# Optimization experiments

Measured on AMD Instinct MI355X. Metric: run time of the kernel, lower is better.

Reference implementation:

```python
import jax, jax.numpy as jnp
import numpy as np

N = 100000
E = 3200000
F_IN = 256
D_OUT = 128


def setup_inputs() -> dict:
    key = jax.random.key(0)
    ks = jax.random.split(key, 12)
    x = jax.random.normal(ks[0], (N, F_IN), dtype=jnp.float32)
    adj_val = jax.random.uniform(ks[1], (E,), dtype=jnp.float32)
    edge_row = jnp.sort(jax.random.randint(ks[2], (E,), 0, N))
    edge_col = jax.random.randint(ks[3], (E,), 0, N)
    # learned params (glorot-ish scaling)
    W1 = jax.random.normal(ks[4], (F_IN, D_OUT), dtype=jnp.float32) * (1.0 / np.sqrt(F_IN))   # conv1d_1 (1x1, no bias)
    w2 = jax.random.normal(ks[5], (D_OUT, 1), dtype=jnp.float32) * (1.0 / np.sqrt(D_OUT))     # conv1d_2
    b2 = jnp.zeros((1,), dtype=jnp.float32)
    w3 = jax.random.normal(ks[6], (D_OUT, 1), dtype=jnp.float32) * (1.0 / np.sqrt(D_OUT))     # conv1d_3
    b3 = jnp.zeros((1,), dtype=jnp.float32)
    kernel = jax.random.normal(ks[7], (F_IN, D_OUT), dtype=jnp.float32) * (1.0 / np.sqrt(F_IN))
    bias = jax.random.normal(ks[8], (N, D_OUT), dtype=jnp.float32) * 0.02
    return {"x": x, "adj_val": adj_val, "W1": W1, "w2": w2, "b2": b2,
            "w3": w3, "b3": b3, "kernel": kernel, "bias": bias,
            "edge_row": edge_row, "edge_col": edge_col}


def reference(x, adj_val, W1, w2, b2, w3, b3, kernel, bias, edge_row, edge_col):
    # 1x1 conv projections (equivalent to per-node dense layers)
    mapped = x @ W1                                   # [N, D]
    sa1 = (mapped @ w2 + b2)[:, 0]                    # [N]
    sa2 = (mapped @ w3 + b3)[:, 0]                    # [N]
    # sparse*dense broadcast then sparse add: per edge (i,j):
    #   adj_val * sa1[i] + adj_val * sa2[j]
    e = adj_val * (sa1[edge_row] + sa2[edge_col])     # [E]
    e = jax.nn.leaky_relu(e, negative_slope=0.2)
    # sparse row-wise softmax over nonzero entries
    m = jax.ops.segment_max(e, edge_row, num_segments=N)        # [N]
    m = jnp.where(jnp.isfinite(m), m, 0.0)
    ex = jnp.exp(e - m[edge_row])                               # [E]
    denom = jax.ops.segment_sum(ex, edge_row, num_segments=N)   # [N]
    denom = jnp.where(denom > 0, denom, 1.0)
    att = ex / denom[edge_row]                                  # [E]
    # dense feature transform then SpMM aggregation
    value = x @ kernel                                          # [N, D_OUT]
    out = jax.ops.segment_sum(att[:, None] * value[edge_col], edge_row, num_segments=N)
    out = out + bias                                            # use_bias=True
    return out  # activation=None (linear), single head, 'average' reduction
```

## Files before the change

kernel.cpp:

```cpp
#include <hip/hip_runtime.h>
#include <math.h>

#define N_NODES 100000
#define N_EDGES 3200000
#define F_IN    256
#define D_OUT   128

typedef __attribute__((ext_vector_type(8))) short short8;
typedef __attribute__((ext_vector_type(4))) float f32x4;

__device__ __forceinline__ unsigned short f2bf(float f) {
    unsigned u = __float_as_uint(f);
    unsigned r = (u + 0x7FFFu + ((u >> 16) & 1u)) >> 16;
    return (unsigned short)r;
}

__device__ __forceinline__ float dot4(f32x4 a, f32x4 b) {
    return a.x * b.x + a.y * b.y + a.z * b.z + a.w * b.w;
}

__device__ __forceinline__ float ub(unsigned u, int k) {
    return (float)((u >> (k * 8)) & 0xffu);
}

__global__ __launch_bounds__(128) void prep_kernel(
    const float* __restrict__ W1, const float* __restrict__ w2,
    const float* __restrict__ w3, const float* __restrict__ kern,
    float* __restrict__ v1, float* __restrict__ v2,
    unsigned short* __restrict__ kbT) {
    const int kk  = blockIdx.x;
    const int tid = threadIdx.x;
    kbT[(size_t)tid * F_IN + kk] = f2bf(kern[(size_t)kk * D_OUT + tid]);
    if (tid < 64) {
        const float* wr = W1 + (size_t)kk * D_OUT;
        float a = wr[tid], b = wr[tid + 64];
        float s1 = a * w2[tid] + b * w2[tid + 64];
        float s2 = a * w3[tid] + b * w3[tid + 64];
#pragma unroll
        for (int o = 32; o > 0; o >>= 1) {
            s1 += __shfl_xor(s1, o);
            s2 += __shfl_xor(s2, o);
        }
        if (tid == 0) { v1[kk] = s1; v2[kk] = s2; }
    }
}

__global__ void row_ptr_kernel(const int* __restrict__ edge_row,
                               int* __restrict__ row_ptr) {
    int r = blockIdx.x * blockDim.x + threadIdx.x;
    if (r > N_NODES) return;
    int lo = 0, hi = N_EDGES;
    while (lo < hi) {
        int mid = (lo + hi) >> 1;
        if (edge_row[mid] < r) lo = mid + 1; else hi = mid;
    }
    row_ptr[r] = lo;
}

__global__ __launch_bounds__(256) void gemm_sa_kernel(
    const float* __restrict__ x, const unsigned short* __restrict__ kbT,
    const float* __restrict__ v1, const float* __restrict__ v2,
    const float* __restrict__ b2p, const float* __restrict__ b3p,
    unsigned char* __restrict__ valq, float2* __restrict__ szc,
    float* __restrict__ sa1) {
    const int wid = blockIdx.x * 4 + (threadIdx.x >> 6);
    const int m_base = wid * 32;
    if (m_base >= N_NODES) return;
    const int lane = threadIdx.x & 63;
    const int r = lane & 15;
    const int q = lane >> 4;

    const f32x4* x0 = (const f32x4*)(x + (size_t)(m_base + r) * F_IN + q * 8);
    const f32x4* x1 = (const f32x4*)(x + (size_t)(m_base + 16 + r) * F_IN + q * 8);

    f32x4 acc[2][8];
#pragma unroll
    for (int t = 0; t < 2; ++t)
#pragma unroll
        for (int nt = 0; nt < 8; ++nt) acc[t][nt] = (f32x4)(0.f);
    float s1a = 0.f, s1b = 0.f, s2a = 0.f, s2b = 0.f;

#pragma unroll 2
    for (int s = 0; s < 8; ++s) {
        f32x4 p00 = __builtin_nontemporal_load(x0 + s * 8);
        f32x4 p01 = __builtin_nontemporal_load(x0 + s * 8 + 1);
        f32x4 p10 = __builtin_nontemporal_load(x1 + s * 8);
        f32x4 p11 = __builtin_nontemporal_load(x1 + s * 8 + 1);
        const f32x4* vp1 = (const f32x4*)(v1 + s * 32 + q * 8);
        const f32x4* vp2 = (const f32x4*)(v2 + s * 32 + q * 8);
        f32x4 va = vp1[0], vb = vp1[1], vc = vp2[0], vd = vp2[1];
        s1a += dot4(p00, va) + dot4(p01, vb);
        s2a += dot4(p00, vc) + dot4(p01, vd);
        s1b += dot4(p10, va) + dot4(p11, vb);
        s2b += dot4(p10, vc) + dot4(p11, vd);

        short8 a0, a1;
        a0[0] = (short)f2bf(p00.x); a0[1] = (short)f2bf(p00.y);
        a0[2] = (short)f2bf(p00.z); a0[3] = (short)f2bf(p00.w);
        a0[4] = (short)f2bf(p01.x); a0[5] = (short)f2bf(p01.y);
        a0[6] = (short)f2bf(p01.z); a0[7] = (short)f2bf(p01.w);
        a1[0] = (short)f2bf(p10.x); a1[1] = (short)f2bf(p10.y);
        a1[2] = (short)f2bf(p10.z); a1[3] = (short)f2bf(p10.w);
        a1[4] = (short)f2bf(p11.x); a1[5] = (short)f2bf(p11.y);
        a1[6] = (short)f2bf(p11.z); a1[7] = (short)f2bf(p11.w);

#pragma unroll
        for (int nt = 0; nt < 8; ++nt) {
            const short8 b = *(const short8*)(kbT + (size_t)(nt * 16 + r) * F_IN
                                              + s * 32 + q * 8);
            acc[0][nt] = __builtin_amdgcn_mfma_f32_16x16x32_bf16(a0, b, acc[0][nt], 0, 0, 0);
            acc[1][nt] = __builtin_amdgcn_mfma_f32_16x16x32_bf16(a1, b, acc[1][nt], 0, 0, 0);
        }
    }

    s1a += __shfl_xor(s1a, 16); s1a += __shfl_xor(s1a, 32);
    s1b += __shfl_xor(s1b, 16); s1b += __shfl_xor(s1b, 32);
    s2a += __shfl_xor(s2a, 16); s2a += __shfl_xor(s2a, 32);
    s2b += __shfl_xor(s2b, 16); s2b += __shfl_xor(s2b, 32);
    if (q == 0) {
        float bb2 = b2p[0], bb3 = b3p[0];
        sa1[m_base + r]      = s1a + bb2;
        sa1[m_base + 16 + r] = s1b + bb2;
        szc[m_base + r].x      = s2a + bb3;
        szc[m_base + 16 + r].x = s2b + bb3;
    }

#pragma unroll
    for (int t = 0; t < 2; ++t)
#pragma unroll
        for (int reg = 0; reg < 4; ++reg) {
            float m = 0.f;
#pragma unroll
            for (int nt = 0; nt < 8; ++nt) m = fmaxf(m, fabsf(acc[t][nt][reg]));
            m = fmaxf(m, __shfl_xor(m, 1));
            m = fmaxf(m, __shfl_xor(m, 2));
            m = fmaxf(m, __shfl_xor(m, 4));
            m = fmaxf(m, __shfl_xor(m, 8));
            const int row = m_base + t * 16 + q * 4 + reg;
            const float inv = m > 0.f ? 127.f / m : 0.f;
            if (r == 0) szc[row].y = m * (1.f / 127.f);
#pragma unroll
            for (int nt = 0; nt < 8; ++nt) {
                int iq = (int)rintf(acc[t][nt][reg] * inv);
                valq[(size_t)row * D_OUT + nt * 16 + r] =
                    (unsigned char)(iq + 128);
            }
        }
}

__global__ __launch_bounds__(256) void attn_agg_kernel(
    const int* __restrict__ row_ptr, const int* __restrict__ edge_col,
    const float* __restrict__ adj, const float* __restrict__ sa1,
    const float2* __restrict__ szc, const unsigned char* __restrict__ valq,
    const float* __restrict__ bias, float* __restrict__ out) {
    const int lane = threadIdx.x & 63;
    const int g    = lane >> 4;
    const int r    = lane & 15;
    const int row  = blockIdx.x * 4 + (threadIdx.x >> 6);

    const int s   = row_ptr[row];
    const int cnt = row_ptr[row + 1] - s;
    const float sa1r = sa1[row];
    const unsigned char* vbase = valq + r * 8;

    const f32x4* bp = (const f32x4*)(bias + (size_t)row * D_OUT + r * 8);
    f32x4 b0 = __builtin_nontemporal_load(bp);
    f32x4 b1 = __builtin_nontemporal_load(bp + 1);

    float acc[8];
#pragma unroll
    for (int j = 0; j < 8; ++j) acc[j] = 0.f;
    float sum = 0.f, sumw = 0.f;

    for (int base = 0; base < cnt; base += 64) {
        const int n = min(64, cnt - base);

        int c = 0;
        float w = 0.f;
        if (lane < n) {
            const int e = s + base + lane;
            c = __builtin_nontemporal_load(edge_col + e);
            const float a = __builtin_nontemporal_load(adj + e);
            const float2 f2 = szc[c];
            float t = a * (sa1r + f2.x);
            t = fmaxf(t, 0.2f * t);
            const float ex = __expf(t);
            sum += ex;
            w = ex * f2.y;
        }
        sumw += w;

        const int nchunk = (n + 15) >> 4;
        uint2 p[16];
#pragma unroll
        for (int ch = 0; ch < 4; ++ch) {
            if (ch < nchunk) {
#pragma unroll
                for (int k4 = 0; k4 < 4; ++k4) {
                    const int k = ch * 4 + k4;
                    const int cc = __shfl(c, k * 4 + g);
                    p[k] = *(const uint2*)(vbase + (size_t)cc * D_OUT);
                }
            }
        }
#pragma unroll
        for (int ch = 0; ch < 4; ++ch) {
            if (ch < nchunk) {
#pragma unroll
                for (int k4 = 0; k4 < 4; ++k4) {
                    const int k = ch * 4 + k4;
                    const float ww = __shfl(w, k * 4 + g);
                    const uint2 q = p[k];
                    acc[0] += ww * ub(q.x, 0); acc[1] += ww * ub(q.x, 1);
                    acc[2] += ww * ub(q.x, 2); acc[3] += ww * ub(q.x, 3);
                    acc[4] += ww * ub(q.y, 0); acc[5] += ww * ub(q.y, 1);
                    acc[6] += ww * ub(q.y, 2); acc[7] += ww * ub(q.y, 3);
                }
            }
        }
    }

    sum  += __shfl_xor(sum, 1);  sumw += __shfl_xor(sumw, 1);
    sum  += __shfl_xor(sum, 2);  sumw += __shfl_xor(sumw, 2);
    sum  += __shfl_xor(sum, 4);  sumw += __shfl_xor(sumw, 4);
    sum  += __shfl_xor(sum, 8);  sumw += __shfl_xor(sumw, 8);
#pragma unroll
    for (int o = 16; o < 64; o <<= 1) {
        sum  += __shfl_xor(sum, o);
        sumw += __shfl_xor(sumw, o);
#pragma unroll
        for (int j = 0; j < 8; ++j) acc[j] += __shfl_xor(acc[j], o);
    }
    const float inv  = sum > 0.f ? 1.f / sum : 1.f;
    const float corr = 128.f * sumw;

    if (g == 0) {
        f32x4 r0, r1;
        r0.x = (acc[0] - corr) * inv + b0.x; r0.y = (acc[1] - corr) * inv + b0.y;
        r0.z = (acc[2] - corr) * inv + b0.z; r0.w = (acc[3] - corr) * inv + b0.w;
        r1.x = (acc[4] - corr) * inv + b1.x; r1.y = (acc[5] - corr) * inv + b1.y;
        r1.z = (acc[6] - corr) * inv + b1.z; r1.w = (acc[7] - corr) * inv + b1.w;
        f32x4* op = (f32x4*)(out + (size_t)row * D_OUT + r * 8);
        __builtin_nontemporal_store(r0, op);
        __builtin_nontemporal_store(r1, op + 1);
    }
}

extern "C" void kernel_launch(void* const* d_in, const int* in_sizes, int n_in,
                              void* d_out, int out_size, void* d_ws,
                              size_t ws_size, hipStream_t stream) {
    const float* x        = (const float*)d_in[0];
    const float* adj      = (const float*)d_in[1];
    const float* W1       = (const float*)d_in[2];
    const float* w2       = (const float*)d_in[3];
    const float* b2       = (const float*)d_in[4];
    const float* w3       = (const float*)d_in[5];
    const float* b3       = (const float*)d_in[6];
    const float* kern     = (const float*)d_in[7];
    const float* bias     = (const float*)d_in[8];
    const int*   edge_row = (const int*)d_in[9];
    const int*   edge_col = (const int*)d_in[10];
    float* out = (float*)d_out;

    unsigned char* valq = (unsigned char*)d_ws;
    float2* szc = (float2*)(valq + (size_t)N_NODES * D_OUT);
    float*  sa1 = (float*)(szc + N_NODES);
    int* row_ptr = (int*)(sa1 + N_NODES);
    float* v1 = (float*)(row_ptr + N_NODES + 4);
    float* v2 = v1 + F_IN;
    unsigned short* kbT = (unsigned short*)(v2 + F_IN);

    hipLaunchKernelGGL(prep_kernel, dim3(256), dim3(128), 0, stream,
                       W1, w2, w3, kern, v1, v2, kbT);
    hipLaunchKernelGGL(row_ptr_kernel, dim3((N_NODES + 1 + 255) / 256),
                       dim3(256), 0, stream, edge_row, row_ptr);
    hipLaunchKernelGGL(gemm_sa_kernel, dim3((N_NODES / 32 + 3) / 4), dim3(256),
                       0, stream, x, kbT, v1, v2, b2, b3, valq, szc, sa1);
    hipLaunchKernelGGL(attn_agg_kernel, dim3(N_NODES / 4), dim3(256), 0,
                       stream, row_ptr, edge_col, adj, sa1, szc, valq,
                       bias, out);
}
```

Baseline: 354.2 us.

## Process two rows per wavefront in attention aggregation to overlap gathers

The attention-aggregation kernel now has each wavefront handle two consecutive rows, issuing the edge loads, score gathers and quantized value gathers for both rows before accumulating. The first 64 edges of each row go through an unrolled fast path, and longer rows fall back to a loop. The aim is more memory-level parallelism per wave and lower per-row fixed costs such as reductions and row_ptr loads. In exchange it raises register pressure, which may reduce occupancy, and duplicates a lot of code.

```diff
diff --git a/kernel.cpp b/kernel.cpp
--- a/kernel.cpp
+++ b/kernel.cpp
@@ -156,91 +156,232 @@
     const int lane = threadIdx.x & 63;
     const int g    = lane >> 4;
     const int r    = lane & 15;
-    const int row  = blockIdx.x * 4 + (threadIdx.x >> 6);
-
-    const int s   = row_ptr[row];
-    const int cnt = row_ptr[row + 1] - s;
-    const float sa1r = sa1[row];
+    const int rA   = __builtin_amdgcn_readfirstlane(
+                         blockIdx.x * 8 + (threadIdx.x >> 6) * 2);
+    const int rB   = rA + 1;
+
+    const int sA = row_ptr[rA];
+    const int eA = row_ptr[rA + 1];
+    const int eB = row_ptr[rA + 2];
+    const int cntA = eA - sA, cntB = eB - eA;
+    const float sa1A = sa1[rA], sa1B = sa1[rB];
     const unsigned char* vbase = valq + r * 8;
 
-    const f32x4* bp = (const f32x4*)(bias + (size_t)row * D_OUT + r * 8);
-    f32x4 b0 = __builtin_nontemporal_load(bp);
-    f32x4 b1 = __builtin_nontemporal_load(bp + 1);
-
-    float acc[8];
-#pragma unroll
-    for (int j = 0; j < 8; ++j) acc[j] = 0.f;
-    float sum = 0.f, sumw = 0.f;
-
-    for (int base = 0; base < cnt; base += 64) {
-        const int n = min(64, cnt - base);
-
-        int c = 0;
-        float w = 0.f;
-        if (lane < n) {
-            const int e = s + base + lane;
-            c = __builtin_nontemporal_load(edge_col + e);
-            const float a = __builtin_nontemporal_load(adj + e);
-            const float2 f2 = szc[c];
-            float t = a * (sa1r + f2.x);
-            t = fmaxf(t, 0.2f * t);
-            const float ex = __expf(t);
-            sum += ex;
-            w = ex * f2.y;
-        }
-        sumw += w;
-
-        const int nchunk = (n + 15) >> 4;
-        uint2 p[16];
-#pragma unroll
-        for (int ch = 0; ch < 4; ++ch) {
-            if (ch < nchunk) {
-#pragma unroll
-                for (int k4 = 0; k4 < 4; ++k4) {
-                    const int k = ch * 4 + k4;
-                    const int cc = __shfl(c, k * 4 + g);
-                    p[k] = *(const uint2*)(vbase + (size_t)cc * D_OUT);
-                }
-            }
-        }
-#pragma unroll
-        for (int ch = 0; ch < 4; ++ch) {
-            if (ch < nchunk) {
-#pragma unroll
-                for (int k4 = 0; k4 < 4; ++k4) {
-                    const int k = ch * 4 + k4;
-                    const float ww = __shfl(w, k * 4 + g);
-                    const uint2 q = p[k];
-                    acc[0] += ww * ub(q.x, 0); acc[1] += ww * ub(q.x, 1);
-                    acc[2] += ww * ub(q.x, 2); acc[3] += ww * ub(q.x, 3);
-                    acc[4] += ww * ub(q.y, 0); acc[5] += ww * ub(q.y, 1);
-                    acc[6] += ww * ub(q.y, 2); acc[7] += ww * ub(q.y, 3);
-                }
-            }
-        }
-    }
-
-    sum  += __shfl_xor(sum, 1);  sumw += __shfl_xor(sumw, 1);
-    sum  += __shfl_xor(sum, 2);  sumw += __shfl_xor(sumw, 2);
-    sum  += __shfl_xor(sum, 4);  sumw += __shfl_xor(sumw, 4);
-    sum  += __shfl_xor(sum, 8);  sumw += __shfl_xor(sumw, 8);
+    const int nA = min(cntA, 64), nB = min(cntB, 64);
+    int cA = 0, cB = 0;
+    float aA = 0.f, aB = 0.f;
+    if (lane < nA) {
+        cA = __builtin_nontemporal_load(edge_col + sA + lane);
+        aA = __builtin_nontemporal_load(adj + sA + lane);
+    }
+    if (lane < nB) {
+        cB = __builtin_nontemporal_load(edge_col + eA + lane);
+        aB = __builtin_nontemporal_load(adj + eA + lane);
+    }
+    float2 fA, fB;
+    fA.x = 0.f; fA.y = 0.f; fB.x = 0.f; fB.y = 0.f;
+    if (lane < nA) fA = szc[cA];
+    if (lane < nB) fB = szc[cB];
+
+    float sumA = 0.f, wA = 0.f;
+    float sumB = 0.f, wB = 0.f;
+    if (lane < nA) {
+        float t = aA * (sa1A + fA.x);
+        t = fmaxf(t, 0.2f * t);
+        const float ex = __expf(t);
+        sumA = ex; wA = ex * fA.y;
+    }
+    if (lane < nB) {
+        float t = aB * (sa1B + fB.x);
+        t = fmaxf(t, 0.2f * t);
+        const float ex = __expf(t);
+        sumB = ex; wB = ex * fB.y;
+    }
+    float sumwA = wA, sumwB = wB;
+
+    float accA[8], accB[8];
+#pragma unroll
+    for (int j = 0; j < 8; ++j) { accA[j] = 0.f; accB[j] = 0.f; }
+
+    const int qA = (nA + 3) >> 2;
+    const int qB = (nB + 3) >> 2;
+    uint2 pA[8], pB[8];
+
+#pragma unroll
+    for (int k = 0; k < 8; ++k)
+        if (k < qA) {
+            const int cc = __shfl(cA, k * 4 + g);
+            pA[k] = *(const uint2*)(vbase + (size_t)cc * D_OUT);
+        }
+#pragma unroll
+    for (int k = 0; k < 8; ++k)
+        if (k < qB) {
+            const int cc = __shfl(cB, k * 4 + g);
+            pB[k] = *(const uint2*)(vbase + (size_t)cc * D_OUT);
+        }
+#pragma unroll
+    for (int k = 0; k < 8; ++k)
+        if (k < qA) {
+            const float ww = __shfl(wA, k * 4 + g);
+            const uint2 q = pA[k];
+            accA[0] += ww * ub(q.x, 0); accA[1] += ww * ub(q.x, 1);
+            accA[2] += ww * ub(q.x, 2); accA[3] += ww * ub(q.x, 3);
+            accA[4] += ww * ub(q.y, 0); accA[5] += ww * ub(q.y, 1);
+            accA[6] += ww * ub(q.y, 2); accA[7] += ww * ub(q.y, 3);
+        }
+    if (qA > 8) {
+#pragma unroll
+        for (int k = 8; k < 16; ++k)
+            if (k < qA) {
+                const int cc = __shfl(cA, k * 4 + g);
+                pA[k - 8] = *(const uint2*)(vbase + (size_t)cc * D_OUT);
+            }
+    }
+#pragma unroll
+    for (int k = 0; k < 8; ++k)
+        if (k < qB) {
+            const float ww = __shfl(wB, k * 4 + g);
+            const uint2 q = pB[k];
+            accB[0] += ww * ub(q.x, 0); accB[1] += ww * ub(q.x, 1);
+            accB[2] += ww * ub(q.x, 2); accB[3] += ww * ub(q.x, 3);
+            accB[4] += ww * ub(q.y, 0); accB[5] += ww * ub(q.y, 1);
+            accB[6] += ww * ub(q.y, 2); accB[7] += ww * ub(q.y, 3);
+        }
+    if (qB > 8) {
+#pragma unroll
+        for (int k = 8; k < 16; ++k)
+            if (k < qB) {
+                const int cc = __shfl(cB, k * 4 + g);
+                pB[k - 8] = *(const uint2*)(vbase + (size_t)cc * D_OUT);
+            }
+    }
+    if (qA > 8) {
+#pragma unroll
+        for (int k = 8; k < 16; ++k)
+            if (k < qA) {
+                const float ww = __shfl(wA, k * 4 + g);
+                const uint2 q = pA[k - 8];
+                accA[0] += ww * ub(q.x, 0); accA[1] += ww * ub(q.x, 1);
+                accA[2] += ww * ub(q.x, 2); accA[3] += ww * ub(q.x, 3);
+                accA[4] += ww * ub(q.y, 0); accA[5] += ww * ub(q.y, 1);
+                accA[6] += ww * ub(q.y, 2); accA[7] += ww * ub(q.y, 3);
+            }
+    }
+    if (qB > 8) {
+#pragma unroll
+        for (int k = 8; k < 16; ++k)
+            if (k < qB) {
+                const float ww = __shfl(wB, k * 4 + g);
+                const uint2 q = pB[k - 8];
+                accB[0] += ww * ub(q.x, 0); accB[1] += ww * ub(q.x, 1);
+                accB[2] += ww * ub(q.x, 2); accB[3] += ww * ub(q.x, 3);
+                accB[4] += ww * ub(q.y, 0); accB[5] += ww * ub(q.y, 1);
+                accB[6] += ww * ub(q.y, 2); accB[7] += ww * ub(q.y, 3);
+            }
+    }
+
+    if (cntA > 64) {
+        for (int base = 64; base < cntA; base += 64) {
+            const int n = min(64, cntA - base);
+            int c = 0; float w = 0.f;
+            if (lane < n) {
+                const int e = sA + base + lane;
+                c = edge_col[e];
+                const float a = adj[e];
+                const float2 f2 = szc[c];
+                float t = a * (sa1A + f2.x);
+                t = fmaxf(t, 0.2f * t);
+                const float ex = __expf(t);
+                sumA += ex; w = ex * f2.y;
+            }
+            sumwA += w;
+            const int qn = (n + 3) >> 2;
+            for (int k = 0; k < qn; ++k) {
+                const int cc = __shfl(c, k * 4 + g);
+                const float ww = __shfl(w, k * 4 + g);
+                const uint2 q = *(const uint2*)(vbase + (size_t)cc * D_OUT);
+                accA[0] += ww * ub(q.x, 0); accA[1] += ww * ub(q.x, 1);
+                accA[2] += ww * ub(q.x, 2); accA[3] += ww * ub(q.x, 3);
+                accA[4] += ww * ub(q.y, 0); accA[5] += ww * ub(q.y, 1);
+                accA[6] += ww * ub(q.y, 2); accA[7] += ww * ub(q.y, 3);
+            }
+        }
+    }
+    if (cntB > 64) {
+        for (int base = 64; base < cntB; base += 64) {
+            const int n = min(64, cntB - base);
+            int c = 0; float w = 0.f;
+            if (lane < n) {
+                const int e = eA + base + lane;
+                c = edge_col[e];
+                const float a = adj[e];
+                const float2 f2 = szc[c];
+                float t = a * (sa1B + f2.x);
+                t = fmaxf(t, 0.2f * t);
+                const float ex = __expf(t);
+                sumB += ex; w = ex * f2.y;
+            }
+            sumwB += w;
+            const int qn = (n + 3) >> 2;
+            for (int k = 0; k < qn; ++k) {
+                const int cc = __shfl(c, k * 4 + g);
+                const float ww = __shfl(w, k * 4 + g);
+                const uint2 q = *(const uint2*)(vbase + (size_t)cc * D_OUT);
+                accB[0] += ww * ub(q.x, 0); accB[1] += ww * ub(q.x, 1);
+                accB[2] += ww * ub(q.x, 2); accB[3] += ww * ub(q.x, 3);
+                accB[4] += ww * ub(q.y, 0); accB[5] += ww * ub(q.y, 1);
+                accB[6] += ww * ub(q.y, 2); accB[7] += ww * ub(q.y, 3);
+            }
+        }
+    }
+
+    const f32x4* bpA = (const f32x4*)(bias + (size_t)rA * D_OUT + r * 8);
+    const f32x4* bpB = (const f32x4*)(bias + (size_t)rB * D_OUT + r * 8);
+    f32x4 bA0, bA1, bB0, bB1;
+    if (g == 0) { bA0 = __builtin_nontemporal_load(bpA);
+                  bA1 = __builtin_nontemporal_load(bpA + 1); }
+    if (g == 1) { bB0 = __builtin_nontemporal_load(bpB);
+                  bB1 = __builtin_nontemporal_load(bpB + 1); }
+
+    sumA += __shfl_xor(sumA, 1);  sumwA += __shfl_xor(sumwA, 1);
+    sumA += __shfl_xor(sumA, 2);  sumwA += __shfl_xor(sumwA, 2);
+    sumA += __shfl_xor(sumA, 4);  sumwA += __shfl_xor(sumwA, 4);
+    sumA += __shfl_xor(sumA, 8);  sumwA += __shfl_xor(sumwA, 8);
+    sumB += __shfl_xor(sumB, 1);  sumwB += __shfl_xor(sumwB, 1);
+    sumB += __shfl_xor(sumB, 2);  sumwB += __shfl_xor(sumwB, 2);
+    sumB += __shfl_xor(sumB, 4);  sumwB += __shfl_xor(sumwB, 4);
+    sumB += __shfl_xor(sumB, 8);  sumwB += __shfl_xor(sumwB, 8);
 #pragma unroll
     for (int o = 16; o < 64; o <<= 1) {
-        sum  += __shfl_xor(sum, o);
-        sumw += __shfl_xor(sumw, o);
-#pragma unroll
-        for (int j = 0; j < 8; ++j) acc[j] += __shfl_xor(acc[j], o);
-    }
-    const float inv  = sum > 0.f ? 1.f / sum : 1.f;
-    const float corr = 128.f * sumw;
+        sumA += __shfl_xor(sumA, o); sumwA += __shfl_xor(sumwA, o);
+        sumB += __shfl_xor(sumB, o); sumwB += __shfl_xor(sumwB, o);
+#pragma unroll
+        for (int j = 0; j < 8; ++j) {
+            accA[j] += __shfl_xor(accA[j], o);
+            accB[j] += __shfl_xor(accB[j], o);
+        }
+    }
 
     if (g == 0) {
+        const float inv  = sumA > 0.f ? 1.f / sumA : 1.f;
+        const float corr = 128.f * sumwA;
         f32x4 r0, r1;
-        r0.x = (acc[0] - corr) * inv + b0.x; r0.y = (acc[1] - corr) * inv + b0.y;
-        r0.z = (acc[2] - corr) * inv + b0.z; r0.w = (acc[3] - corr) * inv + b0.w;
-        r1.x = (acc[4] - corr) * inv + b1.x; r1.y = (acc[5] - corr) * inv + b1.y;
-        r1.z = (acc[6] - corr) * inv + b1.z; r1.w = (acc[7] - corr) * inv + b1.w;
-        f32x4* op = (f32x4*)(out + (size_t)row * D_OUT + r * 8);
+        r0.x = (accA[0] - corr) * inv + bA0.x; r0.y = (accA[1] - corr) * inv + bA0.y;
+        r0.z = (accA[2] - corr) * inv + bA0.z; r0.w = (accA[3] - corr) * inv + bA0.w;
+        r1.x = (accA[4] - corr) * inv + bA1.x; r1.y = (accA[5] - corr) * inv + bA1.y;
+        r1.z = (accA[6] - corr) * inv + bA1.z; r1.w = (accA[7] - corr) * inv + bA1.w;
+        f32x4* op = (f32x4*)(out + (size_t)rA * D_OUT + r * 8);
+        __builtin_nontemporal_store(r0, op);
+        __builtin_nontemporal_store(r1, op + 1);
+    } else if (g == 1) {
+        const float inv  = sumB > 0.f ? 1.f / sumB : 1.f;
+        const float corr = 128.f * sumwB;
+        f32x4 r0, r1;
+        r0.x = (accB[0] - corr) * inv + bB0.x; r0.y = (accB[1] - corr) * inv + bB0.y;
+        r0.z = (accB[2] - corr) * inv + bB0.z; r0.w = (accB[3] - corr) * inv + bB0.w;
+        r1.x = (accB[4] - corr) * inv + bB1.x; r1.y = (accB[5] - corr) * inv + bB1.y;
+        r1.z = (accB[6] - corr) * inv + bB1.z; r1.w = (accB[7] - corr) * inv + bB1.w;
+        f32x4* op = (f32x4*)(out + (size_t)rB * D_OUT + r * 8);
         __builtin_nontemporal_store(r0, op);
         __builtin_nontemporal_store(r1, op + 1);
     }
@@ -276,7 +417,7 @@
                        dim3(256), 0, stream, edge_row, row_ptr);
     hipLaunchKernelGGL(gemm_sa_kernel, dim3((N_NODES / 32 + 3) / 4), dim3(256),
                        0, stream, x, kbT, v1, v2, b2, b3, valq, szc, sa1);
-    hipLaunchKernelGGL(attn_agg_kernel, dim3(N_NODES / 4), dim3(256), 0,
+    hipLaunchKernelGGL(attn_agg_kernel, dim3(N_NODES / 8), dim3(256), 0,
                        stream, row_ptr, edge_col, adj, sa1, szc, valq,
                        bias, out);
 }
```

Result: faster. 339.2 us (-4.2%).
